# Kernel optimization log

Measured on AMD Instinct MI355X. Metric: run time of the kernel, lower is better.

## Reference

```python
import jax, jax.numpy as jnp
import numpy as np

S = 8            # n_internal_streams
N = 2**S - 1     # 255 cliques (all non-empty subsets of streams)
D = 32           # half_dim = consciousness_dim // 2
INPUT_DIM = 512
NUM_ITER = 5
B = 1024


def _configs():
    # binary membership of each clique (non-empty subsets), [N, S]
    return ((np.arange(1, 2**S)[:, None] >> np.arange(S)) & 1).astype(np.float32)


def setup_inputs() -> dict:
    key = jax.random.key(0)
    ks = jax.random.split(key, 10)
    cfg = _configs()
    depths = cfg.sum(-1)
    # topological amplitude init: gaussian profile over clique depth
    center, sigma = S / 2.0, S / 3.0
    prof = np.exp(-((depths - center) ** 2) / (2 * sigma ** 2))
    prof = prof / (np.linalg.norm(prof) + 1e-8)
    psi_A0 = jnp.asarray(np.broadcast_to(prof[None, :, None], (1, N, D)).copy(),
                         jnp.float32) + jax.random.normal(ks[0], (1, N, D)) * 0.01
    inp = {
        'network_state': jax.random.normal(ks[1], (B, INPUT_DIM), jnp.float32),
        'W_streams': jax.random.normal(ks[2], (S * D, INPUT_DIM)) / np.sqrt(INPUT_DIM),
        'b_streams': jnp.zeros((S * D,), jnp.float32),
        'W_A': jax.random.normal(ks[3], (D, D)) / np.sqrt(D),
        'b_A': jnp.zeros((D,), jnp.float32),
        'W_phi': jax.random.normal(ks[4], (D, D)) / np.sqrt(D),
        'b_phi': jnp.zeros((D,), jnp.float32),
        'psi_A0': psi_A0,
        'psi_phi0': jax.random.normal(ks[5], (1, N, D)) * 0.3,
        'W_comp': jax.random.normal(ks[6], (32, N)) / np.sqrt(N),
        'b_comp': jnp.zeros((32,), jnp.float32),
        'W_read': jax.random.normal(ks[7], (2 * D, 32 * D)) / np.sqrt(32 * D),
        'b_read': jnp.zeros((2 * D,), jnp.float32),
        'alpha_kin': jnp.asarray(0.5, jnp.float32),
        'mass_sq': jnp.asarray(0.1, jnp.float32),
        'potential_weight': jnp.asarray(0.3, jnp.float32),
        'input_weight': jnp.asarray(0.5, jnp.float32),
        'evolution_rate': jnp.asarray(0.3, jnp.float32),
        'phase_coupling': jnp.asarray(1.0, jnp.float32),
    }
    return inp


def reference(network_state, W_streams, b_streams, W_A, b_A, W_phi, b_phi,
              psi_A0, psi_phi0, W_comp, b_comp, W_read, b_read,
              alpha_kin, mass_sq, potential_weight, input_weight,
              evolution_rate, phase_coupling):
    cfg = jnp.asarray(_configs())                      # [N,S]
    depths = cfg.sum(-1)                               # [N]
    # Hamming-distance kernel between clique configurations
    Ham = cfg @ (1.0 - cfg).T + (1.0 - cfg) @ cfg.T    # [N,N]
    K = jnp.exp(-Ham / S)
    krow = K.sum(1)                                    # [N]

    Bb = network_state.shape[0]
    feats = (network_state @ W_streams.T + b_streams).reshape(Bb, S, D)
    # clique features: mean of member-stream features
    cf = jnp.einsum('ns,bsd->bnd', cfg, feats) / depths[None, :, None]
    A_input = jax.nn.softplus(cf @ W_A.T + b_A)        # [B,N,D]
    phi_input = jnp.pi * jnp.tanh(cf @ W_phi.T + b_phi)

    A = jax.nn.softplus(jnp.broadcast_to(psi_A0, (Bb, N, D)))
    phi = jnp.broadcast_to(psi_phi0, (Bb, N, D))
    dt = jax.nn.sigmoid(evolution_rate)

    for _ in range(NUM_ITER):
        # laplacian: sum_j K_ij (A_j - A_i) / N  (factorized, same math)
        KA = jnp.einsum('ij,bjd->bid', K, A)
        lap = (KA - krow[None, :, None] * A) / N
        sp, cp = jnp.sin(phi), jnp.cos(phi)
        Ks = jnp.einsum('ij,bjd->bid', K, sp)
        Kc = jnp.einsum('ij,bjd->bid', K, cp)
        # sum_j K_ij A_i sin(phi_j - phi_i) / N
        pc = A * (cp * Ks - sp * Kc) / N
        # nonlocal potential: V_i = sum_j K_ij A_j cos(phi_j - phi_i) / N
        KAc = jnp.einsum('ij,bjd->bid', K, A * cp)
        KAs = jnp.einsum('ij,bjd->bid', K, A * sp)
        V = (cp * KAc + sp * KAs) / N
        input_drive = A_input * jnp.sin(phi_input - phi)
        dA = (alpha_kin * lap + potential_weight * V - mass_sq * A
              + input_weight * (A_input - A))
        A = jax.nn.softplus(A + dt * dA)               # updated A used in dphi
        dphi = alpha_kin * pc / (A + 1e-8) + input_weight * input_drive
        phi = phi + dt * dphi
        # per-clique norm clip to 1
        norms = jnp.maximum(jnp.linalg.norm(A, axis=-1, keepdims=True), 1e-8)
        A = A * jnp.where(norms > 1.0, 1.0 / norms, 1.0)

    A_t = jnp.swapaxes(A, 1, 2)                        # [B,D,N]
    Ac = jax.nn.relu(A_t @ W_comp.T + b_comp)          # [B,D,32]
    ro = Ac.reshape(Bb, -1) @ W_read.T + b_read        # [B,2D]
    amplitude = jax.nn.softplus(ro[:, :D])
    phase = jnp.tanh(ro[:, D:] * phase_coupling) * jnp.pi
    psi = (amplitude * jnp.cos(phase)).astype(jnp.complex64) + 1j * (amplitude * jnp.sin(phase)).astype(jnp.complex64)
    return psi, amplitude, phase
```

## Files before the change

kernel.cpp:

```cpp
#include <hip/hip_runtime.h>
#include <math.h>

#define PI_F   3.14159265358979f
#define QF     0.88249690258459546f
#define INV255 (1.0f/255.0f)

__device__ __forceinline__ float softplus_f(float x){
    return fmaxf(x, 0.0f) + __logf(1.0f + __expf(-fabsf(x)));
}
__device__ __forceinline__ float tanh_fast(float x){
    const float e = __expf(2.0f*x);
    return fmaf(-2.0f, __builtin_amdgcn_rcpf(e + 1.0f), 1.0f);
}

template<int CTRL>
__device__ __forceinline__ float dppmov(float x){
    return __int_as_float(__builtin_amdgcn_mov_dpp(__float_as_int(x), CTRL, 0xF, 0xF, false));
}
__device__ __forceinline__ float lxor1 (float x){ return dppmov<0xB1>(x);  }
__device__ __forceinline__ float lxor2 (float x){ return dppmov<0x4E>(x);  }
__device__ __forceinline__ float lxor8 (float x){ return dppmov<0x128>(x); }
__device__ __forceinline__ float lxor4 (float x){ return __int_as_float(__builtin_amdgcn_ds_swizzle(__float_as_int(x), 0x101F)); }
__device__ __forceinline__ float lxor16(float x){ return __int_as_float(__builtin_amdgcn_ds_swizzle(__float_as_int(x), 0x401F)); }
__device__ __forceinline__ float lxor32(float x){ return __shfl_xor(x, 32, 64); }

template<int CTRL>
__device__ __forceinline__ float dppadd(float v){
    return v + __int_as_float(__builtin_amdgcn_update_dpp(0, __float_as_int(v), CTRL, 0xF, 0xF, true));
}
__device__ __forceinline__ float wave_sum63(float v){
    v = dppadd<0x111>(v);
    v = dppadd<0x112>(v);
    v = dppadd<0x114>(v);
    v = dppadd<0x118>(v);
    v = dppadd<0x142>(v);
    v = dppadd<0x143>(v);
    return v;
}

template<int NA>
__device__ __forceinline__ void bflyN(float (&x)[NA][4]){
    const float qv = QF;
    #pragma unroll
    for (int a = 0; a < NA; a++){
        #pragma unroll
        for (int r = 0; r < 4; r++) x[a][r] = fmaf(lxor1 (x[a][r]), qv, x[a][r]);
    }
    #pragma unroll
    for (int a = 0; a < NA; a++){
        #pragma unroll
        for (int r = 0; r < 4; r++) x[a][r] = fmaf(lxor2 (x[a][r]), qv, x[a][r]);
    }
    #pragma unroll
    for (int a = 0; a < NA; a++){
        #pragma unroll
        for (int r = 0; r < 4; r++) x[a][r] = fmaf(lxor8 (x[a][r]), qv, x[a][r]);
    }
    #pragma unroll
    for (int a = 0; a < NA; a++){
        #pragma unroll
        for (int r = 0; r < 4; r++) x[a][r] = fmaf(lxor4 (x[a][r]), qv, x[a][r]);
    }
    #pragma unroll
    for (int a = 0; a < NA; a++){
        #pragma unroll
        for (int r = 0; r < 4; r++) x[a][r] = fmaf(lxor16(x[a][r]), qv, x[a][r]);
    }
    #pragma unroll
    for (int a = 0; a < NA; a++){
        #pragma unroll
        for (int r = 0; r < 4; r++) x[a][r] = fmaf(lxor32(x[a][r]), qv, x[a][r]);
    }
    #pragma unroll
    for (int a = 0; a < NA; a++){
        float t0 = x[a][0], t2 = x[a][2];
        x[a][0] = fmaf(QF, x[a][1], x[a][0]);
        x[a][1] = fmaf(QF, t0,      x[a][1]);
        x[a][2] = fmaf(QF, x[a][3], x[a][2]);
        x[a][3] = fmaf(QF, t2,      x[a][3]);
        t0 = x[a][0]; float t1 = x[a][1];
        x[a][0] = fmaf(QF, x[a][2], x[a][0]);
        x[a][1] = fmaf(QF, x[a][3], x[a][1]);
        x[a][2] = fmaf(QF, t0,      x[a][2]);
        x[a][3] = fmaf(QF, t1,      x[a][3]);
    }
}

__global__ __launch_bounds__(256) void prep_kernel(
        const float* __restrict__ Ws,    const float* __restrict__ psiA0,
        const float* __restrict__ psiP0, const float* __restrict__ p_alpha,
        const float* __restrict__ p_msq, const float* __restrict__ p_pw,
        const float* __restrict__ p_iw,  const float* __restrict__ p_evo,
        float* __restrict__ WsT,  float* __restrict__ Xc,  float* __restrict__ P0c,
        float* __restrict__ S0c,  float* __restrict__ C0c, float* __restrict__ F0c)
{
    if (blockIdx.x < 32){
        __shared__ float tile[64][65];
        const int rt = blockIdx.x & 3, ct = blockIdx.x >> 2;
        const int r0 = rt*64, c0t = ct*64;
        const int tx = threadIdx.x & 63, ty = threadIdx.x >> 6;
        #pragma unroll
        for (int k = 0; k < 16; k++){
            const int row = ty*16 + k;
            tile[row][tx] = Ws[(r0+row)*512 + c0t + tx];
        }
        __syncthreads();
        #pragma unroll
        for (int k = 0; k < 16; k++){
            const int row = ty*16 + k;
            WsT[(c0t+row)*256 + r0 + tx] = tile[tx][row];
        }
        return;
    }
    const int tid = threadIdx.x;
    const int w = tid >> 6, l = tid & 63;
    const float alpha = p_alpha[0], msq = p_msq[0], pw = p_pw[0], iw = p_iw[0];
    const float dt   = 1.0f / (1.0f + __expf(-p_evo[0]));
    const float dta  = dt * alpha * INV255;
    const float dtpw = dt * pw * INV255;
    const float c0   = 1.0f - dt * (msq + iw);
    const float m0 = (l == 0) ? 0.0f : 1.0f;
    int nn[4]; float krow[4];
    float c18;
    { const float t1 = 1.0f + QF, t2 = t1*t1, t4 = t2*t2; c18 = t4*t4; }
    #pragma unroll
    for (int r = 0; r < 4; r++){
        nn[r] = l + 64*r;
        krow[r] = c18 - __expf(-0.125f * (float)__popc(nn[r]));
    }
    #pragma unroll
    for (int dd = 0; dd < 8; dd++){
        const int d = w*8 + dd;
        float A0[4], ph0[4], sp[4], cp[4];
        float x[5][4];
        #pragma unroll
        for (int r = 0; r < 4; r++){
            const int n = nn[r];
            A0[r]  = (n > 0) ? softplus_f(psiA0[(n-1)*32 + d]) : 0.0f;
            ph0[r] = (n > 0) ? psiP0[(n-1)*32 + d] : 0.0f;
            sp[r] = __sinf(ph0[r]); cp[r] = __cosf(ph0[r]);
            const float mk = (r == 0) ? m0 : 1.0f;
            const float xa = A0[r] * mk;
            x[0][r] = xa;
            x[1][r] = sp[r] * mk;
            x[2][r] = cp[r] * mk;
            x[3][r] = xa * cp[r];
            x[4][r] = xa * sp[r];
        }
        bflyN<5>(x);
        #pragma unroll
        for (int r = 0; r < 4; r++){
            const float Ao   = A0[r];
            const float lapp = fmaf(-krow[r], Ao, x[0][r]);
            const float Vp   = fmaf(cp[r], x[3][r], sp[r]*x[4][r]);
            const float Pp   = fmaf(-sp[r], x[2][r], cp[r]*x[1][r]);
            float X = c0 * Ao;
            X = fmaf(dta,  lapp, X);
            X = fmaf(dtpw, Vp,   X);
            const int idx = d*256 + nn[r];
            Xc[idx]  = X;
            P0c[idx] = dta * Ao * Pp;
            S0c[idx] = sp[r];
            C0c[idx] = cp[r];
            F0c[idx] = ph0[r];
        }
    }
}

template<bool USET>
__global__ __launch_bounds__(256) void fused_kernel(
        const float* __restrict__ ns,
        const float* __restrict__ Ws,
        const float* __restrict__ WsT,
        const float* __restrict__ bs,
        const float* __restrict__ WA,
        const float* __restrict__ bA,
        const float* __restrict__ WP,
        const float* __restrict__ bP,
        const float* __restrict__ psiA0,
        const float* __restrict__ psiP0,
        const float* __restrict__ Xc,
        const float* __restrict__ P0c,
        const float* __restrict__ S0c,
        const float* __restrict__ C0c,
        const float* __restrict__ F0c,
        const float* __restrict__ Wcomp,
        const float* __restrict__ bcomp,
        const float* __restrict__ Wread,
        const float* __restrict__ bread,
        const float* __restrict__ p_alpha, const float* __restrict__ p_msq,
        const float* __restrict__ p_pw,    const float* __restrict__ p_iw,
        const float* __restrict__ p_evo,   const float* __restrict__ p_pcpl,
        float* __restrict__ out, int Bb)
{
    __shared__ __align__(16) float nsb[512];
    __shared__ __align__(16) float fe[256];
    __shared__ __align__(16) float hA[256];
    __shared__ __align__(16) float hP[256];
    __shared__ __align__(16) float red[2][1024];
    __shared__ __align__(16) float ac[1024];
    __shared__ __align__(16) float rop[256];

    const int b   = blockIdx.x;
    const int tid = threadIdx.x;
    const int w   = tid >> 6, l = tid & 63;

    const float alpha = p_alpha[0], msq = p_msq[0], pw = p_pw[0], iw = p_iw[0];
    const float pcpl  = p_pcpl[0];
    const float dt    = 1.0f / (1.0f + __expf(-p_evo[0]));
    const float dta  = dt * alpha * INV255;
    const float dtpw = dt * pw * INV255;
    const float c0   = 1.0f - dt * (msq + iw);
    const float dtiw = dt * iw;

    nsb[tid]       = ns[b*512 + tid];
    nsb[tid + 256] = ns[b*512 + 256 + tid];
    __syncthreads();
    if (USET){
        float f = bs[tid];
        const float4* nb4 = (const float4*)nsb;
        #pragma unroll 8
        for (int j4 = 0; j4 < 128; j4++){
            const float4 nv = nb4[j4];
            const float* col = WsT + j4*1024 + tid;
            f = fmaf(col[0],   nv.x, f);
            f = fmaf(col[256], nv.y, f);
            f = fmaf(col[512], nv.z, f);
            f = fmaf(col[768], nv.w, f);
        }
        fe[tid] = f;
    } else {
        float f = bs[tid];
        const float4* wr  = (const float4*)(Ws + tid*512);
        const float4* nb4 = (const float4*)nsb;
        #pragma unroll 8
        for (int i = 0; i < 128; i++){
            const float4 wv = wr[i], nv = nb4[i];
            f = fmaf(wv.x, nv.x, f); f = fmaf(wv.y, nv.y, f);
            f = fmaf(wv.z, nv.z, f); f = fmaf(wv.w, nv.w, f);
        }
        fe[tid] = f;
    }
    __syncthreads();
    {
        const int s = tid >> 5, d = tid & 31;
        float a = 0.0f, p = 0.0f;
        #pragma unroll 8
        for (int dp = 0; dp < 32; dp++){
            const float fv = fe[s*32 + dp];
            a = fmaf(WA[d*32 + dp], fv, a);
            p = fmaf(WP[d*32 + dp], fv, p);
        }
        hA[tid] = a; hP[tid] = p;
    }
    __syncthreads();

    int   nn[4];
    float krow[4], rdep[4];
    const float m0 = (l == 0) ? 0.0f : 1.0f;
    float c18;
    { const float t1 = 1.0f + QF, t2 = t1*t1, t4 = t2*t2; c18 = t4*t4; }
    #pragma unroll
    for (int r = 0; r < 4; r++){
        nn[r] = l + 64*r;
        const int pop = __popc(nn[r]);
        krow[r]  = c18 - __expf(-0.125f * (float)pop);
        rdep[r]  = 1.0f / (float)(pop ? pop : 1);
    }

    float A[8][4], phi[8][4], CAp[8][4], Dsp[8][4], Dcp[8][4];
    float nrm0[4] = {0.f, 0.f, 0.f, 0.f};

    #pragma unroll
    for (int dd = 0; dd < 8; dd++){
        const int d = w*8 + dd;
        const float bAd = bA[d], bPd = bP[d];
        float gA_[8], gP_[8];
        #pragma unroll
        for (int s = 0; s < 8; s++){ gA_[s] = hA[s*32 + d]; gP_[s] = hP[s*32 + d]; }
        #pragma unroll
        for (int r = 0; r < 4; r++){
            float sA = 0.0f, sP = 0.0f;
            #pragma unroll
            for (int s = 0; s < 8; s++){
                if ((nn[r] >> s) & 1){ sA += gA_[s]; sP += gP_[s]; }
            }
            const float uA  = fmaf(sA, rdep[r], bAd);
            const float uP  = fmaf(sP, rdep[r], bPd);
            const float Ain = softplus_f(uA);
            const float pin = PI_F * tanh_fast(uP);
            const float si = __sinf(pin), ci = __cosf(pin);
            const float ca = dtiw * Ain;
            CAp[dd][r] = ca; Dsp[dd][r] = ca * si; Dcp[dd][r] = ca * ci;
            if (USET){
                const int idx = d*256 + nn[r];
                const float An = softplus_f(Xc[idx] + ca);
                const float rr = __builtin_amdgcn_rcpf(An + 1e-8f);
                float pb = fmaf(Dsp[dd][r], C0c[idx], F0c[idx]);
                pb = fmaf(-Dcp[dd][r], S0c[idx], pb);
                phi[dd][r] = fmaf(P0c[idx], rr, pb);
                A[dd][r]   = An;
                nrm0[r]    = fmaf(An, An, nrm0[r]);
            } else {
                const int nm1 = (nn[r] > 0) ? (nn[r] - 1) : 0;
                A[dd][r]   = softplus_f(psiA0[nm1*32 + d]);
                phi[dd][r] = psiP0[nm1*32 + d];
            }
        }
    }

    if (USET){
        #pragma unroll
        for (int r = 0; r < 4; r++) red[0][w*256 + nn[r]] = nrm0[r];
        __syncthreads();
        float scl[4];
        #pragma unroll
        for (int r = 0; r < 4; r++){
            const float t = red[0][nn[r]] + red[0][256 + nn[r]]
                          + red[0][512 + nn[r]] + red[0][768 + nn[r]];
            scl[r] = (t > 1.0f) ? rsqrtf(t) : 1.0f;
        }
        #pragma unroll
        for (int dd = 0; dd < 8; dd++)
            #pragma unroll
            for (int r = 0; r < 4; r++) A[dd][r] *= scl[r];
    }

    const int NFULL = USET ? 3 : 4;
    for (int it = 0; it < NFULL; it++){
        const int pbuf = USET ? ((it + 1) & 1) : (it & 1);
        float nrm[4] = {0.f, 0.f, 0.f, 0.f};
        #pragma unroll
        for (int dd = 0; dd < 8; dd++){
            float sp[4], cp[4];
            float x[5][4];
            {
                sp[0] = __sinf(phi[dd][0]); cp[0] = __cosf(phi[dd][0]);
                const float xa = A[dd][0] * m0;
                x[0][0] = xa;
                x[1][0] = sp[0] * m0;
                x[2][0] = cp[0] * m0;
                x[3][0] = xa * cp[0];
                x[4][0] = xa * sp[0];
            }
            #pragma unroll
            for (int r = 1; r < 4; r++){
                sp[r] = __sinf(phi[dd][r]); cp[r] = __cosf(phi[dd][r]);
                const float xa = A[dd][r];
                x[0][r] = xa;
                x[1][r] = sp[r];
                x[2][r] = cp[r];
                x[3][r] = xa * cp[r];
                x[4][r] = xa * sp[r];
            }
            bflyN<5>(x);
            #pragma unroll
            for (int r = 0; r < 4; r++){
                const float Ao   = A[dd][r];
                const float lapp = fmaf(-krow[r], Ao, x[0][r]);
                const float Vp   = fmaf(cp[r], x[3][r], sp[r]*x[4][r]);
                float Aarg = fmaf(c0, Ao, CAp[dd][r]);
                Aarg = fmaf(dta,  lapp, Aarg);
                Aarg = fmaf(dtpw, Vp,   Aarg);
                const float An = softplus_f(Aarg);
                const float Pp = fmaf(-sp[r], x[2][r], cp[r]*x[1][r]);
                const float rr = __builtin_amdgcn_rcpf(An + 1e-8f);
                float pb = fmaf(Dsp[dd][r], cp[r], phi[dd][r]);
                pb = fmaf(-Dcp[dd][r], sp[r], pb);
                phi[dd][r] = fmaf(dta*Ao, Pp*rr, pb);
                A[dd][r]   = An;
                nrm[r]     = fmaf(An, An, nrm[r]);
            }
        }
        #pragma unroll
        for (int r = 0; r < 4; r++) red[pbuf][w*256 + nn[r]] = nrm[r];
        __syncthreads();
        float scl[4];
        #pragma unroll
        for (int r = 0; r < 4; r++){
            const float t = red[pbuf][nn[r]] + red[pbuf][256 + nn[r]]
                          + red[pbuf][512 + nn[r]] + red[pbuf][768 + nn[r]];
            scl[r] = (t > 1.0f) ? rsqrtf(t) : 1.0f;
        }
        #pragma unroll
        for (int dd = 0; dd < 8; dd++)
            #pragma unroll
            for (int r = 0; r < 4; r++) A[dd][r] *= scl[r];
    }

    {
        float nrm[4] = {0.f, 0.f, 0.f, 0.f};
        #pragma unroll
        for (int dd = 0; dd < 8; dd++){
            float sp[4], cp[4];
            float y[3][4];
            {
                sp[0] = __sinf(phi[dd][0]); cp[0] = __cosf(phi[dd][0]);
                const float xa = A[dd][0] * m0;
                y[0][0] = xa;
                y[1][0] = xa * cp[0];
                y[2][0] = xa * sp[0];
            }
            #pragma unroll
            for (int r = 1; r < 4; r++){
                sp[r] = __sinf(phi[dd][r]); cp[r] = __cosf(phi[dd][r]);
                const float xa = A[dd][r];
                y[0][r] = xa;
                y[1][r] = xa * cp[r];
                y[2][r] = xa * sp[r];
            }
            bflyN<3>(y);
            #pragma unroll
            for (int r = 0; r < 4; r++){
                const float Ao   = A[dd][r];
                const float lapp = fmaf(-krow[r], Ao, y[0][r]);
                const float Vp   = fmaf(cp[r], y[1][r], sp[r]*y[2][r]);
                float Aarg = fmaf(c0, Ao, CAp[dd][r]);
                Aarg = fmaf(dta,  lapp, Aarg);
                Aarg = fmaf(dtpw, Vp,   Aarg);
                const float An = softplus_f(Aarg);
                A[dd][r]   = An;
                nrm[r]     = fmaf(An, An, nrm[r]);
            }
        }
        #pragma unroll
        for (int r = 0; r < 4; r++) red[0][w*256 + nn[r]] = nrm[r];
        __syncthreads();
        float scl[4];
        #pragma unroll
        for (int r = 0; r < 4; r++){
            const float t = red[0][nn[r]] + red[0][256 + nn[r]]
                          + red[0][512 + nn[r]] + red[0][768 + nn[r]];
            scl[r] = (t > 1.0f) ? rsqrtf(t) : 1.0f;
        }
        #pragma unroll
        for (int dd = 0; dd < 8; dd++)
            #pragma unroll
            for (int r = 0; r < 4; r++) A[dd][r] *= scl[r];
    }

    #pragma unroll
    for (int dd = 0; dd < 8; dd++) A[dd][0] *= m0;

    for (int c = 0; c < 32; c++){
        float wv[4];
        #pragma unroll
        for (int r = 0; r < 4; r++){
            const int idx = c*255 + nn[r] - 1;
            wv[r] = Wcomp[idx < 0 ? 0 : idx];
        }
        const float bc = bcomp[c];
        #pragma unroll
        for (int dd = 0; dd < 8; dd++){
            float v = wv[0] * A[dd][0];
            v = fmaf(wv[1], A[dd][1], v);
            v = fmaf(wv[2], A[dd][2], v);
            v = fmaf(wv[3], A[dd][3], v);
            v = wave_sum63(v);
            if (l == 63)
                ac[(w*8 + dd)*32 + c] = fmaxf(v + bc, 0.0f);
        }
    }
    __syncthreads();

    {
        const int k = tid >> 2, part = tid & 3;
        const float4* Wr4 = (const float4*)Wread + k*256;
        const float4* ac4 = (const float4*)ac;
        float s = 0.0f;
        #pragma unroll 4
        for (int jj = 0; jj < 64; jj++){
            const int j4 = part + 4*jj;
            const float4 wv = Wr4[j4];
            const float4 av = ac4[j4];
            s = fmaf(wv.x, av.x, s); s = fmaf(wv.y, av.y, s);
            s = fmaf(wv.z, av.z, s); s = fmaf(wv.w, av.w, s);
        }
        rop[tid] = s;
    }
    __syncthreads();
    if (tid < 32){
        const float ra = rop[tid*4] + rop[tid*4+1] + rop[tid*4+2] + rop[tid*4+3] + bread[tid];
        const int   t2 = tid + 32;
        const float rp = rop[t2*4] + rop[t2*4+1] + rop[t2*4+2] + rop[t2*4+3] + bread[t2];
        const float amp = softplus_f(ra);
        const float ph  = PI_F * tanhf(rp * pcpl);
        const float cph = __cosf(ph);
        const int o = b*32 + tid;
        out[o]         = amp * cph;
        out[Bb*32 + o] = amp;
        out[Bb*64 + o] = ph;
    }
}

extern "C" void kernel_launch(void* const* d_in, const int* in_sizes, int n_in,
                              void* d_out, int out_size, void* d_ws, size_t ws_size,
                              hipStream_t stream) {
    const float* ns      = (const float*)d_in[0];
    const float* Ws      = (const float*)d_in[1];
    const float* bs      = (const float*)d_in[2];
    const float* WA      = (const float*)d_in[3];
    const float* bA      = (const float*)d_in[4];
    const float* WP      = (const float*)d_in[5];
    const float* bP      = (const float*)d_in[6];
    const float* psiA0   = (const float*)d_in[7];
    const float* psiP0   = (const float*)d_in[8];
    const float* Wcomp   = (const float*)d_in[9];
    const float* bcomp   = (const float*)d_in[10];
    const float* Wread   = (const float*)d_in[11];
    const float* bread   = (const float*)d_in[12];
    const float* p_alpha = (const float*)d_in[13];
    const float* p_msq   = (const float*)d_in[14];
    const float* p_pw    = (const float*)d_in[15];
    const float* p_iw    = (const float*)d_in[16];
    const float* p_evo   = (const float*)d_in[17];
    const float* p_pcpl  = (const float*)d_in[18];

    const int Bb = in_sizes[0] / 512;

    const size_t need = (size_t)(512*256 + 5*32*256) * sizeof(float);
    if (ws_size >= need){
        float* WsT = (float*)d_ws;
        float* Xc  = WsT + 512*256;
        float* P0c = Xc  + 32*256;
        float* S0c = P0c + 32*256;
        float* C0c = S0c + 32*256;
        float* F0c = C0c + 32*256;
        prep_kernel<<<33, 256, 0, stream>>>(Ws, psiA0, psiP0,
                                            p_alpha, p_msq, p_pw, p_iw, p_evo,
                                            WsT, Xc, P0c, S0c, C0c, F0c);
        fused_kernel<true><<<Bb, 256, 0, stream>>>(ns, Ws, WsT, bs, WA, bA, WP, bP,
                                                   psiA0, psiP0, Xc, P0c, S0c, C0c, F0c,
                                                   Wcomp, bcomp, Wread, bread,
                                                   p_alpha, p_msq, p_pw, p_iw,
                                                   p_evo, p_pcpl, (float*)d_out, Bb);
    } else {
        fused_kernel<false><<<Bb, 256, 0, stream>>>(ns, Ws, nullptr, bs, WA, bA, WP, bP,
                                                    psiA0, psiP0,
                                                    nullptr, nullptr, nullptr, nullptr, nullptr,
                                                    Wcomp, bcomp, Wread, bread,
                                                    p_alpha, p_msq, p_pw, p_iw,
                                                    p_evo, p_pcpl, (float*)d_out, Bb);
    }
}
```

Measured before the change: 309.6 us.

## Stage A in LDS and compute clique compression as per-thread dot products

After: 357.1 us. +15.3%, slower.

```diff
diff --git a/kernel.cpp b/kernel.cpp
--- a/kernel.cpp
+++ b/kernel.cpp
@@ -88,11 +88,13 @@
 
 __global__ __launch_bounds__(256) void prep_kernel(
         const float* __restrict__ Ws,    const float* __restrict__ psiA0,
-        const float* __restrict__ psiP0, const float* __restrict__ p_alpha,
+        const float* __restrict__ psiP0, const float* __restrict__ Wcomp,
+        const float* __restrict__ p_alpha,
         const float* __restrict__ p_msq, const float* __restrict__ p_pw,
         const float* __restrict__ p_iw,  const float* __restrict__ p_evo,
         float* __restrict__ WsT,  float* __restrict__ Xc,  float* __restrict__ P0c,
-        float* __restrict__ S0c,  float* __restrict__ C0c, float* __restrict__ F0c)
+        float* __restrict__ S0c,  float* __restrict__ C0c, float* __restrict__ F0c,
+        float* __restrict__ WcompP)
 {
     if (blockIdx.x < 32){
         __shared__ float tile[64][65];
@@ -109,6 +111,13 @@
         for (int k = 0; k < 16; k++){
             const int row = ty*16 + k;
             WsT[(c0t+row)*256 + r0 + tx] = tile[tx][row];
+        }
+        return;
+    }
+    if (blockIdx.x == 33){
+        for (int i = threadIdx.x; i < 32*256; i += 256){
+            const int c = i >> 8, n = i & 255;
+            WcompP[i] = (n > 0) ? Wcomp[c*255 + n - 1] : 0.0f;
         }
         return;
     }
@@ -184,6 +193,7 @@
         const float* __restrict__ S0c,
         const float* __restrict__ C0c,
         const float* __restrict__ F0c,
+        const float* __restrict__ WcompP,
         const float* __restrict__ Wcomp,
         const float* __restrict__ bcomp,
         const float* __restrict__ Wread,
@@ -193,13 +203,15 @@
         const float* __restrict__ p_evo,   const float* __restrict__ p_pcpl,
         float* __restrict__ out, int Bb)
 {
-    __shared__ __align__(16) float nsb[512];
-    __shared__ __align__(16) float fe[256];
-    __shared__ __align__(16) float hA[256];
-    __shared__ __align__(16) float hP[256];
-    __shared__ __align__(16) float red[2][1024];
-    __shared__ __align__(16) float ac[1024];
-    __shared__ __align__(16) float rop[256];
+    __shared__ __align__(16) float smem[9344];
+    float* nsb = smem;
+    float* fe  = smem + 512;
+    float* hA  = smem + 768;
+    float* hP  = smem + 1024;
+    float* red = smem + 1280;
+    float* aLDS = smem;
+    float* ac  = smem + 8320;
+    float* rop = smem;
 
     const int b   = blockIdx.x;
     const int tid = threadIdx.x;
@@ -311,13 +323,13 @@
 
     if (USET){
         #pragma unroll
-        for (int r = 0; r < 4; r++) red[0][w*256 + nn[r]] = nrm0[r];
+        for (int r = 0; r < 4; r++) red[w*256 + nn[r]] = nrm0[r];
         __syncthreads();
         float scl[4];
         #pragma unroll
         for (int r = 0; r < 4; r++){
-            const float t = red[0][nn[r]] + red[0][256 + nn[r]]
-                          + red[0][512 + nn[r]] + red[0][768 + nn[r]];
+            const float t = red[nn[r]] + red[256 + nn[r]]
+                          + red[512 + nn[r]] + red[768 + nn[r]];
             scl[r] = (t > 1.0f) ? rsqrtf(t) : 1.0f;
         }
         #pragma unroll
@@ -329,6 +341,7 @@
     const int NFULL = USET ? 3 : 4;
     for (int it = 0; it < NFULL; it++){
         const int pbuf = USET ? ((it + 1) & 1) : (it & 1);
+        float* rb = red + pbuf*1024;
         float nrm[4] = {0.f, 0.f, 0.f, 0.f};
         #pragma unroll
         for (int dd = 0; dd < 8; dd++){
@@ -373,13 +386,13 @@
             }
         }
         #pragma unroll
-        for (int r = 0; r < 4; r++) red[pbuf][w*256 + nn[r]] = nrm[r];
+        for (int r = 0; r < 4; r++) rb[w*256 + nn[r]] = nrm[r];
         __syncthreads();
         float scl[4];
         #pragma unroll
         for (int r = 0; r < 4; r++){
-            const float t = red[pbuf][nn[r]] + red[pbuf][256 + nn[r]]
-                          + red[pbuf][512 + nn[r]] + red[pbuf][768 + nn[r]];
+            const float t = rb[nn[r]] + rb[256 + nn[r]]
+                          + rb[512 + nn[r]] + rb[768 + nn[r]];
             scl[r] = (t > 1.0f) ? rsqrtf(t) : 1.0f;
         }
         #pragma unroll
@@ -424,13 +437,13 @@
             }
         }
         #pragma unroll
-        for (int r = 0; r < 4; r++) red[0][w*256 + nn[r]] = nrm[r];
+        for (int r = 0; r < 4; r++) red[w*256 + nn[r]] = nrm[r];
         __syncthreads();
         float scl[4];
         #pragma unroll
         for (int r = 0; r < 4; r++){
-            const float t = red[0][nn[r]] + red[0][256 + nn[r]]
-                          + red[0][512 + nn[r]] + red[0][768 + nn[r]];
+            const float t = red[nn[r]] + red[256 + nn[r]]
+                          + red[512 + nn[r]] + red[768 + nn[r]];
             scl[r] = (t > 1.0f) ? rsqrtf(t) : 1.0f;
         }
         #pragma unroll
@@ -442,26 +455,68 @@
     #pragma unroll
     for (int dd = 0; dd < 8; dd++) A[dd][0] *= m0;
 
-    for (int c = 0; c < 32; c++){
-        float wv[4];
-        #pragma unroll
-        for (int r = 0; r < 4; r++){
-            const int idx = c*255 + nn[r] - 1;
-            wv[r] = Wcomp[idx < 0 ? 0 : idx];
-        }
-        const float bc = bcomp[c];
+    if (USET){
+        __syncthreads();
         #pragma unroll
         for (int dd = 0; dd < 8; dd++){
-            float v = wv[0] * A[dd][0];
-            v = fmaf(wv[1], A[dd][1], v);
-            v = fmaf(wv[2], A[dd][2], v);
-            v = fmaf(wv[3], A[dd][3], v);
-            v = wave_sum63(v);
-            if (l == 63)
-                ac[(w*8 + dd)*32 + c] = fmaxf(v + bc, 0.0f);
-        }
-    }
-    __syncthreads();
+            const int d = w*8 + dd;
+            #pragma unroll
+            for (int r = 0; r < 4; r++) aLDS[d*260 + nn[r]] = A[dd][r];
+        }
+        __syncthreads();
+        {
+            const int d  = tid >> 3;
+            const int ci = (tid & 7) * 4;
+            const float4* arow = (const float4*)(aLDS + d*260);
+            const float4* w0 = (const float4*)(WcompP + (ci+0)*256);
+            const float4* w1 = (const float4*)(WcompP + (ci+1)*256);
+            const float4* w2 = (const float4*)(WcompP + (ci+2)*256);
+            const float4* w3 = (const float4*)(WcompP + (ci+3)*256);
+            float s0 = 0.f, s1 = 0.f, s2 = 0.f, s3 = 0.f;
+            #pragma unroll 8
+            for (int j = 0; j < 64; j++){
+                const float4 av = arow[j];
+                const float4 v0 = w0[j], v1 = w1[j], v2 = w2[j], v3 = w3[j];
+                s0 = fmaf(av.x, v0.x, s0); s0 = fmaf(av.y, v0.y, s0);
+                s0 = fmaf(av.z, v0.z, s0); s0 = fmaf(av.w, v0.w, s0);
+                s1 = fmaf(av.x, v1.x, s1); s1 = fmaf(av.y, v1.y, s1);
+                s1 = fmaf(av.z, v1.z, s1); s1 = fmaf(av.w, v1.w, s1);
+                s2 = fmaf(av.x, v2.x, s2); s2 = fmaf(av.y, v2.y, s2);
+                s2 = fmaf(av.z, v2.z, s2); s2 = fmaf(av.w, v2.w, s2);
+                s3 = fmaf(av.x, v3.x, s3); s3 = fmaf(av.y, v3.y, s3);
+                s3 = fmaf(av.z, v3.z, s3); s3 = fmaf(av.w, v3.w, s3);
+            }
+            const float4 bc4 = *(const float4*)(bcomp + ci);
+            float4 o;
+            o.x = fmaxf(s0 + bc4.x, 0.0f);
+            o.y = fmaxf(s1 + bc4.y, 0.0f);
+            o.z = fmaxf(s2 + bc4.z, 0.0f);
+            o.w = fmaxf(s3 + bc4.w, 0.0f);
+            *(float4*)(ac + d*32 + ci) = o;
+        }
+        __syncthreads();
+    } else {
+        for (int c = 0; c < 32; c++){
+            float wv[4];
+            #pragma unroll
+            for (int r = 0; r < 4; r++){
+                const int idx = c*255 + nn[r] - 1;
+                wv[r] = Wcomp[idx < 0 ? 0 : idx];
+            }
+            const float bc = bcomp[c];
+            #pragma unroll
+            for (int dd = 0; dd < 8; dd++){
+                float v = wv[0] * A[dd][0];
+                v = fmaf(wv[1], A[dd][1], v);
+                v = fmaf(wv[2], A[dd][2], v);
+                v = fmaf(wv[3], A[dd][3], v);
+                v = wave_sum63(v);
+                if (l == 63)
+                    ac[(w*8 + dd)*32 + c] = fmaxf(v + bc, 0.0f);
+            }
+        }
+        __syncthreads();
+    }
 
     {
         const int k = tid >> 2, part = tid & 3;
@@ -476,6 +531,7 @@
             s = fmaf(wv.x, av.x, s); s = fmaf(wv.y, av.y, s);
             s = fmaf(wv.z, av.z, s); s = fmaf(wv.w, av.w, s);
         }
+        __syncthreads();
         rop[tid] = s;
     }
     __syncthreads();
@@ -518,27 +574,28 @@
 
     const int Bb = in_sizes[0] / 512;
 
-    const size_t need = (size_t)(512*256 + 5*32*256) * sizeof(float);
+    const size_t need = (size_t)(512*256 + 5*32*256 + 32*256) * sizeof(float);
     if (ws_size >= need){
-        float* WsT = (float*)d_ws;
-        float* Xc  = WsT + 512*256;
-        float* P0c = Xc  + 32*256;
-        float* S0c = P0c + 32*256;
-        float* C0c = S0c + 32*256;
-        float* F0c = C0c + 32*256;
-        prep_kernel<<<33, 256, 0, stream>>>(Ws, psiA0, psiP0,
+        float* WsT    = (float*)d_ws;
+        float* Xc     = WsT + 512*256;
+        float* P0c    = Xc  + 32*256;
+        float* S0c    = P0c + 32*256;
+        float* C0c    = S0c + 32*256;
+        float* F0c    = C0c + 32*256;
+        float* WcompP = F0c + 32*256;
+        prep_kernel<<<34, 256, 0, stream>>>(Ws, psiA0, psiP0, Wcomp,
                                             p_alpha, p_msq, p_pw, p_iw, p_evo,
-                                            WsT, Xc, P0c, S0c, C0c, F0c);
+                                            WsT, Xc, P0c, S0c, C0c, F0c, WcompP);
         fused_kernel<true><<<Bb, 256, 0, stream>>>(ns, Ws, WsT, bs, WA, bA, WP, bP,
                                                    psiA0, psiP0, Xc, P0c, S0c, C0c, F0c,
-                                                   Wcomp, bcomp, Wread, bread,
+                                                   WcompP, Wcomp, bcomp, Wread, bread,
                                                    p_alpha, p_msq, p_pw, p_iw,
                                                    p_evo, p_pcpl, (float*)d_out, Bb);
     } else {
         fused_kernel<false><<<Bb, 256, 0, stream>>>(ns, Ws, nullptr, bs, WA, bA, WP, bP,
                                                     psiA0, psiP0,
                                                     nullptr, nullptr, nullptr, nullptr, nullptr,
-                                                    Wcomp, bcomp, Wread, bread,
+                                                    nullptr, Wcomp, bcomp, Wread, bread,
                                                     p_alpha, p_msq, p_pw, p_iw,
                                                     p_evo, p_pcpl, (float*)d_out, Bb);
     }
```
